# Optimization experiments

Measured on AMD Instinct MI355X. Metric: run time of the kernel, lower is better.

## Reference

```python
import jax, jax.numpy as jnp
import numpy as np
import math

B, H, W = 32, 512, 512
BS = 8
QUALITY = 50.0  # __scale_quality(75) = 200 - 2*75


def _make_dctmtx(bs=BS):
    m = np.empty((bs, bs), dtype=np.float32)
    for j in range(bs):
        for i in range(bs):
            if i == 0:
                m[i, j] = 1.0 / math.sqrt(bs)
            else:
                m[i, j] = math.sqrt(2.0 / bs) * math.cos(math.pi * (2 * j + 1) * i / (2 * bs))
    return jnp.asarray(m)


def _make_quantize():
    qY = np.array([[16,11,10,16,24,40,51,61],[12,12,14,19,26,58,60,55],
                   [14,13,16,24,40,57,69,56],[14,17,22,29,51,87,80,62],
                   [18,22,37,56,68,109,103,77],[24,35,55,64,81,104,113,92],
                   [49,64,78,87,103,121,120,101],[72,92,95,98,112,100,103,99]], dtype=np.float32) / 255.0
    qC = np.array([[17,18,24,47,99,99,99,99],[18,21,26,66,99,99,99,99],
                   [24,26,56,99,99,99,99,99],[47,66,99,99,99,99,99,99],
                   [99,99,99,99,99,99,99,99],[99,99,99,99,99,99,99,99],
                   [99,99,99,99,99,99,99,99],[99,99,99,99,99,99,99,99]], dtype=np.float32) / 255.0
    return jnp.asarray(np.stack([qY, qC, qC], axis=0))


def setup_inputs() -> dict:
    key = jax.random.key(0)
    x = jax.random.uniform(key, (B, 3, H, W), dtype=jnp.float32)
    return {"input": x, "quantize": _make_quantize(), "dctmtx": _make_dctmtx()}


def reference(input, quantize, dctmtx):
    bs = BS
    b, c, h, w = input.shape
    dt = input.dtype
    rgb = 255.0 * input
    # rgb -> ycbcr (3x3 color transform, offset cb/cr by 128, clamp)
    xf = jnp.array([[0.299, 0.587, 0.114],
                    [-0.168735892, -0.331264108, 0.5],
                    [0.5, -0.418687589, -0.081312411]], dtype=dt)
    off = jnp.array([0.0, 128.0, 128.0], dtype=dt)[None, :, None, None]
    ycbcr = jnp.clip(jnp.einsum('bchw,kc->bkhw', rgb, xf) + off, 0.0, 255.0)
    # 2x2 chroma subsample: replace Cb/Cr by 2x2 block means (Y untouched)
    yc = ycbcr[:, :1]
    cc = ycbcr[:, 1:].reshape(b, 2, h // 2, 2, w // 2, 2)
    cm = jnp.mean(cc, axis=(3, 5), keepdims=True)
    cc = jnp.broadcast_to(cm, cc.shape).reshape(b, 2, h, w)
    sample = jnp.concatenate([yc, cc], axis=1) - 128.0
    # extract 8x8 blocks -> [b, h/bs, w/bs, 3, bs, bs]
    blocks = sample.reshape(b, 3, h // bs, bs, w // bs, bs).transpose(0, 2, 4, 1, 3, 5)
    # 2D DCT: D @ X @ D^T
    dcts = jnp.einsum('ij,bhwcjk,lk->bhwcil', dctmtx, blocks, dctmtx)
    # quality-scaled quant table (broadcasts [3,8,8] over blocks)
    q = jnp.round(jnp.clip(jnp.round((jnp.round(quantize * 255.0) * QUALITY + 50.0) / 100.0), 1.0, 255.0))
    comp = jnp.round(dcts / q)
    decomp = jnp.round(comp * jax.lax.stop_gradient(q))
    # IDCT: D^T @ X @ D
    idcts = jnp.einsum('ji,bhwcjk,kl->bhwcil', dctmtx, decomp, dctmtx)
    # merge blocks back -> [b,3,h,w]
    ycbcr2 = idcts.transpose(0, 3, 1, 4, 2, 5).reshape(b, 3, h, w) + 128.0
    # ycbcr -> rgb
    xf2 = jnp.array([[1.0, 0.0, 1.402],
                     [1.0, -0.344136286, -0.714136286],
                     [1.0, 1.772, 0.0]], dtype=dt)
    im = ycbcr2 - off
    rgb2 = jnp.clip(jnp.einsum('bchw,kc->bkhw', im, xf2), 0.0, 255.0)
    return jnp.round(rgb2) / 255.0
```

## Files before the change

kernel.cpp:

```cpp
#include <hip/hip_runtime.h>

#define IN_H 512
#define IN_W 512


__global__ __launch_bounds__(256, 2) void jpeg_kernel(
    const float* __restrict__ in, const float* __restrict__ qz,
    const float* __restrict__ dmtx, float* __restrict__ out)
{
    __shared__ __align__(16) unsigned char smem[39168];
    double*  Ys  = (double*) (smem);
    double*  CbS = (double*) (smem + 17408);
    double*  CrS = (double*) (smem + 22016);
    float*   Zt  = (float*)  (smem + 26624);
    double2* qt  = (double2*)(smem + 35328);
    double*  Dd  = (double*) (smem + 38784);
    float*   Dh  = (float*)  (smem + 39040);

    const int t   = threadIdx.x;
    const int blk = blockIdx.x;
    const int b   = blk >> 7;
    const int rr  = blk & 127;
    const int row0 = (rr >> 1) << 3;
    const int col0 = (rr & 1) << 8;
    const int chs = IN_H * IN_W;

    if (t < 192) {
        const int c = t >> 6, i = (t >> 3) & 7, l = t & 7;
        double v  = (double)qz[t];
        double t1 = rint((rint(v * 255.0) * 50.0 + 50.0) / 100.0);
        double q  = fmin(fmax(t1, 1.0), 255.0);
        qt[(c * 8 + l) * 9 + i] = make_double2(1.0 / q, q);
    }
    if (t < 32) {
        float dv = dmtx[(t >> 2) * 8 + (t & 3)];
        Dd[t] = (double)dv;
        Dh[t] = dv;
    }

    const int s  = t >> 6;
    const int c4 = t & 63;
    {
        const int base = ((b * 3) * IN_H + row0 + 2 * s) * IN_W + col0 + 4 * c4;
        float4 ra = *(const float4*)(in + base);
        float4 rb = *(const float4*)(in + base + IN_W);
        float4 ga = *(const float4*)(in + base + chs);
        float4 gb = *(const float4*)(in + base + chs + IN_W);
        float4 ba = *(const float4*)(in + base + 2 * chs);
        float4 bb = *(const float4*)(in + base + 2 * chs + IN_W);

        float rA[2][4] = {{ra.x,ra.y,ra.z,ra.w},{rb.x,rb.y,rb.z,rb.w}};
        float gA[2][4] = {{ga.x,ga.y,ga.z,ga.w},{gb.x,gb.y,gb.z,gb.w}};
        float bA[2][4] = {{ba.x,ba.y,ba.z,ba.w},{bb.x,bb.y,bb.z,bb.w}};

        double yv[2][4], cbv[2][4], crv[2][4];
        #pragma unroll
        for (int p = 0; p < 2; ++p) {
            #pragma unroll
            for (int k = 0; k < 4; ++k) {
                double R = 255.0 * (double)rA[p][k];
                double G = 255.0 * (double)gA[p][k];
                double B = 255.0 * (double)bA[p][k];
                double y  =  0.299*R + 0.587*G + 0.114*B;
                double cb = -0.168735892*R - 0.331264108*G + 0.5*B + 128.0;
                double cr =  0.5*R - 0.418687589*G - 0.081312411*B + 128.0;
                yv[p][k]  = fmin(fmax(y , 0.0), 255.0) - 128.0;
                cbv[p][k] = fmin(fmax(cb, 0.0), 255.0);
                crv[p][k] = fmin(fmax(cr, 0.0), 255.0);
            }
        }
        const int tile = c4 >> 1, half = c4 & 1;
        #pragma unroll
        for (int p = 0; p < 2; ++p) {
            double* yp = &Ys[tile * 68 + (2*s + p) * 8 + 4 * half];
            *(double2*)(yp)     = make_double2(yv[p][0], yv[p][1]);
            *(double2*)(yp + 2) = make_double2(yv[p][2], yv[p][3]);
        }
        double m0 = (cbv[0][0]+cbv[0][1]+cbv[1][0]+cbv[1][1])*0.25 - 128.0;
        double m1 = (cbv[0][2]+cbv[0][3]+cbv[1][2]+cbv[1][3])*0.25 - 128.0;
        *(double2*)&CbS[tile * 18 + s * 4 + 2 * half] = make_double2(m0, m1);
        double n0 = (crv[0][0]+crv[0][1]+crv[1][0]+crv[1][1])*0.25 - 128.0;
        double n1 = (crv[0][2]+crv[0][3]+crv[1][2]+crv[1][3])*0.25 - 128.0;
        *(double2*)&CrS[tile * 18 + s * 4 + 2 * half] = make_double2(n0, n1);
    }
    __syncthreads();

    const int q8 = t >> 3;
    const int l  = t & 7;
    double dl0, dl1, dl2, dl3;
    {
        double2 dA = *(const double2*)&Dd[l * 4];
        double2 dB = *(const double2*)&Dd[l * 4 + 2];
        dl0 = dA.x; dl1 = dA.y; dl2 = dB.x; dl3 = dB.y;
    }
    const double sgn  = (l & 1) ? -1.0 : 1.0;
    const double dl01 = dl0 + dl1, dl23 = dl2 + dl3;
    float dcol[8];
    {
        const int   lc = (l < 4) ? l : 7 - l;
        #pragma unroll
        for (int k = 0; k < 8; ++k) {
            float dv = Dh[k * 4 + lc];
            dcol[k] = ((k & 1) && (l >= 4)) ? -dv : dv;
        }
    }

    float acc[3][8];

    #pragma unroll
    for (int c = 0; c < 3; ++c) {
        double e2[4], o2[4];
        if (c == 0) {
            const double* base = &Ys[q8 * 68];
            #pragma unroll
            for (int m = 0; m < 4; ++m) {
                double tp[2];
                #pragma unroll
                for (int h = 0; h < 2; ++h) {
                    const double* p = base + (h ? (7 - m) : m) * 8;
                    double2 a0 = *(const double2*)(p);
                    double2 a1 = *(const double2*)(p + 2);
                    double2 a2 = *(const double2*)(p + 4);
                    double2 a3 = *(const double2*)(p + 6);
                    double v0 = fma(sgn, a3.y, a0.x);
                    double v1 = fma(sgn, a3.x, a0.y);
                    double v2 = fma(sgn, a2.y, a1.x);
                    double v3 = fma(sgn, a2.x, a1.y);
                    tp[h] = dl0*v0 + dl1*v1 + dl2*v2 + dl3*v3;
                }
                e2[m] = tp[0] + tp[1];
                o2[m] = tp[0] - tp[1];
            }
        } else {
            const double* base = ((c == 1) ? CbS : CrS) + q8 * 18;
            double u[4];
            #pragma unroll
            for (int j2 = 0; j2 < 4; ++j2) {
                double2 a0 = *(const double2*)(base + j2 * 4);
                double2 a1 = *(const double2*)(base + j2 * 4 + 2);
                u[j2] = dl01 * fma(sgn, a1.y, a0.x) + dl23 * fma(sgn, a1.x, a0.y);
            }
            e2[0] = e2[1] = u[0] + u[3];  o2[0] = o2[1] = u[0] - u[3];
            e2[2] = e2[3] = u[1] + u[2];  o2[2] = o2[3] = u[1] - u[2];
        }

        const double2* dd2  = (const double2*)Dd;
        const double2* qrow = &qt[(c * 8 + l) * 9];
        float* zp = &Zt[q8 * 68 + l * 8];
        #pragma unroll
        for (int hh = 0; hh < 2; ++hh) {
            float zo[4];
            #pragma unroll
            for (int ii = 0; ii < 4; ++ii) {
                const int i = hh * 4 + ii;
                double2 dA = dd2[i * 2], dB = dd2[i * 2 + 1];
                double a64 = (i & 1)
                    ? dA.x*o2[0] + dA.y*o2[1] + dB.x*o2[2] + dB.y*o2[3]
                    : dA.x*e2[0] + dA.y*e2[1] + dB.x*e2[2] + dB.y*e2[3];
                double2 qe = qrow[i];
                zo[ii] = (float)(rint(a64 * qe.x) * qe.y);
            }
            *(float4*)(zp + 4 * hh) = make_float4(zo[0], zo[1], zo[2], zo[3]);
        }
        __syncthreads();

        float w[8] = {0,0,0,0,0,0,0,0};
        const float* zb = &Zt[q8 * 68];
        #pragma unroll
        for (int k = 0; k < 8; ++k) {
            float4 z0 = *(const float4*)(zb + k * 8);
            float4 z1 = *(const float4*)(zb + k * 8 + 4);
            float dk = dcol[k];
            w[0] += z0.x*dk; w[1] += z0.y*dk; w[2] += z0.z*dk; w[3] += z0.w*dk;
            w[4] += z1.x*dk; w[5] += z1.y*dk; w[6] += z1.z*dk; w[7] += z1.w*dk;
        }
        const float4* dh4 = (const float4*)Dh;
        float se[4] = {0,0,0,0}, so[4] = {0,0,0,0};
        #pragma unroll
        for (int j = 0; j < 8; j += 2) {
            float4 de = dh4[j], dq = dh4[j + 1];
            se[0] += de.x*w[j];   se[1] += de.y*w[j];   se[2] += de.z*w[j];   se[3] += de.w*w[j];
            so[0] += dq.x*w[j+1]; so[1] += dq.y*w[j+1]; so[2] += dq.z*w[j+1]; so[3] += dq.w*w[j+1];
        }
        #pragma unroll
        for (int i2 = 0; i2 < 4; ++i2) {
            acc[c][i2]     = se[i2] + so[i2];
            acc[c][7 - i2] = se[i2] - so[i2];
        }
        if (c < 2) __syncthreads();
    }

    #pragma unroll
    for (int i = 0; i < 8; ++i) {
        float im0 = acc[0][i] + 128.0f;
        float im1 = acc[1][i];
        float im2 = acc[2][i];
        float R  = fminf(fmaxf(im0 + 1.402f*im2, 0.0f), 255.0f);
        float G  = fminf(fmaxf(im0 - 0.344136286f*im1 - 0.714136286f*im2, 0.0f), 255.0f);
        float Bv = fminf(fmaxf(im0 + 1.772f*im1, 0.0f), 255.0f);
        const int base = ((b * 3) * IN_H + row0 + i) * IN_W + col0 + t;
        out[base]           = rintf(R)  * (1.0f/255.0f);
        out[base + chs]     = rintf(G)  * (1.0f/255.0f);
        out[base + 2*chs]   = rintf(Bv) * (1.0f/255.0f);
    }
}

extern "C" void kernel_launch(void* const* d_in, const int* in_sizes, int n_in,
                              void* d_out, int out_size, void* d_ws, size_t ws_size,
                              hipStream_t stream) {
    (void)in_sizes; (void)n_in; (void)out_size; (void)d_ws; (void)ws_size;
    const float* in  = (const float*)d_in[0];
    const float* qz  = (const float*)d_in[1];
    const float* dm  = (const float*)d_in[2];
    float* out = (float*)d_out;
    dim3 grid(4096), blk(256);
    hipLaunchKernelGGL(jpeg_kernel, grid, blk, 0, stream, in, qz, dm, out);
}
```

Baseline: 187.2 us.

## Keep IDCT per 8x8 tile within one wave and vectorize output stores

```diff
diff --git a/kernel.cpp b/kernel.cpp
--- a/kernel.cpp
+++ b/kernel.cpp
@@ -12,7 +12,7 @@
     double*  Ys  = (double*) (smem);
     double*  CbS = (double*) (smem + 17408);
     double*  CrS = (double*) (smem + 22016);
-    float*   Zt  = (float*)  (smem + 26624);
+    float*   Vt  = (float*)  (smem + 26624);
     double2* qt  = (double2*)(smem + 35328);
     double*  Dd  = (double*) (smem + 38784);
     float*   Dh  = (float*)  (smem + 39040);
@@ -95,17 +95,12 @@
     }
     const double sgn  = (l & 1) ? -1.0 : 1.0;
     const double dl01 = dl0 + dl1, dl23 = dl2 + dl3;
-    float dcol[8];
-    {
-        const int   lc = (l < 4) ? l : 7 - l;
-        #pragma unroll
-        for (int k = 0; k < 8; ++k) {
-            float dv = Dh[k * 4 + lc];
-            dcol[k] = ((k & 1) && (l >= 4)) ? -dv : dv;
-        }
-    }
+    const float4* dh4p = (const float4*)Dh;
+    float4 d0 = dh4p[0], d1 = dh4p[1], d2 = dh4p[2], d3 = dh4p[3];
+    float4 d4 = dh4p[4], d5 = dh4p[5], d6 = dh4p[6], d7 = dh4p[7];
 
     float acc[3][8];
+    float* vtw = &Vt[q8 * 68];
 
     #pragma unroll
     for (int c = 0; c < 3; ++c) {
@@ -133,75 +128,98 @@
             }
         } else {
             const double* base = ((c == 1) ? CbS : CrS) + q8 * 18;
-            double u[4];
+            double u4[4];
             #pragma unroll
             for (int j2 = 0; j2 < 4; ++j2) {
                 double2 a0 = *(const double2*)(base + j2 * 4);
                 double2 a1 = *(const double2*)(base + j2 * 4 + 2);
-                u[j2] = dl01 * fma(sgn, a1.y, a0.x) + dl23 * fma(sgn, a1.x, a0.y);
-            }
-            e2[0] = e2[1] = u[0] + u[3];  o2[0] = o2[1] = u[0] - u[3];
-            e2[2] = e2[3] = u[1] + u[2];  o2[2] = o2[3] = u[1] - u[2];
-        }
-
-        const double2* dd2  = (const double2*)Dd;
-        const double2* qrow = &qt[(c * 8 + l) * 9];
-        float* zp = &Zt[q8 * 68 + l * 8];
-        #pragma unroll
-        for (int hh = 0; hh < 2; ++hh) {
-            float zo[4];
-            #pragma unroll
-            for (int ii = 0; ii < 4; ++ii) {
-                const int i = hh * 4 + ii;
+                u4[j2] = dl01 * fma(sgn, a1.y, a0.x) + dl23 * fma(sgn, a1.x, a0.y);
+            }
+            e2[0] = e2[1] = u4[0] + u4[3];  o2[0] = o2[1] = u4[0] - u4[3];
+            e2[2] = e2[3] = u4[1] + u4[2];  o2[2] = o2[3] = u4[1] - u4[2];
+        }
+
+        float zo[8];
+        {
+            const double2* dd2  = (const double2*)Dd;
+            const double2* qrow = &qt[(c * 8 + l) * 9];
+            #pragma unroll
+            for (int i = 0; i < 8; ++i) {
                 double2 dA = dd2[i * 2], dB = dd2[i * 2 + 1];
                 double a64 = (i & 1)
                     ? dA.x*o2[0] + dA.y*o2[1] + dB.x*o2[2] + dB.y*o2[3]
                     : dA.x*e2[0] + dA.y*e2[1] + dB.x*e2[2] + dB.y*e2[3];
                 double2 qe = qrow[i];
-                zo[ii] = (float)(rint(a64 * qe.x) * qe.y);
-            }
-            *(float4*)(zp + 4 * hh) = make_float4(zo[0], zo[1], zo[2], zo[3]);
-        }
-        __syncthreads();
-
-        float w[8] = {0,0,0,0,0,0,0,0};
-        const float* zb = &Zt[q8 * 68];
-        #pragma unroll
-        for (int k = 0; k < 8; ++k) {
-            float4 z0 = *(const float4*)(zb + k * 8);
-            float4 z1 = *(const float4*)(zb + k * 8 + 4);
-            float dk = dcol[k];
-            w[0] += z0.x*dk; w[1] += z0.y*dk; w[2] += z0.z*dk; w[3] += z0.w*dk;
-            w[4] += z1.x*dk; w[5] += z1.y*dk; w[6] += z1.z*dk; w[7] += z1.w*dk;
-        }
-        const float4* dh4 = (const float4*)Dh;
-        float se[4] = {0,0,0,0}, so[4] = {0,0,0,0};
-        #pragma unroll
-        for (int j = 0; j < 8; j += 2) {
-            float4 de = dh4[j], dq = dh4[j + 1];
-            se[0] += de.x*w[j];   se[1] += de.y*w[j];   se[2] += de.z*w[j];   se[3] += de.w*w[j];
-            so[0] += dq.x*w[j+1]; so[1] += dq.y*w[j+1]; so[2] += dq.z*w[j+1]; so[3] += dq.w*w[j+1];
-        }
-        #pragma unroll
-        for (int i2 = 0; i2 < 4; ++i2) {
-            acc[c][i2]     = se[i2] + so[i2];
-            acc[c][7 - i2] = se[i2] - so[i2];
-        }
-        if (c < 2) __syncthreads();
-    }
-
-    #pragma unroll
-    for (int i = 0; i < 8; ++i) {
-        float im0 = acc[0][i] + 128.0f;
-        float im1 = acc[1][i];
-        float im2 = acc[2][i];
-        float R  = fminf(fmaxf(im0 + 1.402f*im2, 0.0f), 255.0f);
-        float G  = fminf(fmaxf(im0 - 0.344136286f*im1 - 0.714136286f*im2, 0.0f), 255.0f);
-        float Bv = fminf(fmaxf(im0 + 1.772f*im1, 0.0f), 255.0f);
-        const int base = ((b * 3) * IN_H + row0 + i) * IN_W + col0 + t;
-        out[base]           = rintf(R)  * (1.0f/255.0f);
-        out[base + chs]     = rintf(G)  * (1.0f/255.0f);
-        out[base + 2*chs]   = rintf(Bv) * (1.0f/255.0f);
+                zo[i] = (float)(rint(a64 * qe.x) * qe.y);
+            }
+        }
+
+        float u[8];
+        {
+            float se0 = zo[0]*d0.x + zo[2]*d2.x + zo[4]*d4.x + zo[6]*d6.x;
+            float se1 = zo[0]*d0.y + zo[2]*d2.y + zo[4]*d4.y + zo[6]*d6.y;
+            float se2 = zo[0]*d0.z + zo[2]*d2.z + zo[4]*d4.z + zo[6]*d6.z;
+            float se3 = zo[0]*d0.w + zo[2]*d2.w + zo[4]*d4.w + zo[6]*d6.w;
+            float so0 = zo[1]*d1.x + zo[3]*d3.x + zo[5]*d5.x + zo[7]*d7.x;
+            float so1 = zo[1]*d1.y + zo[3]*d3.y + zo[5]*d5.y + zo[7]*d7.y;
+            float so2 = zo[1]*d1.z + zo[3]*d3.z + zo[5]*d5.z + zo[7]*d7.z;
+            float so3 = zo[1]*d1.w + zo[3]*d3.w + zo[5]*d5.w + zo[7]*d7.w;
+            u[0]=se0+so0; u[7]=se0-so0;
+            u[1]=se1+so1; u[6]=se1-so1;
+            u[2]=se2+so2; u[5]=se2-so2;
+            u[3]=se3+so3; u[4]=se3-so3;
+        }
+
+        #pragma unroll
+        for (int x = 0; x < 8; ++x) vtw[x * 8 + l] = u[x];
+        __builtin_amdgcn_wave_barrier();
+        float w2[8];
+        {
+            const float* vr = vtw + l * 8;
+            float4 wa = *(const float4*)(vr);
+            float4 wb = *(const float4*)(vr + 4);
+            w2[0]=wa.x; w2[1]=wa.y; w2[2]=wa.z; w2[3]=wa.w;
+            w2[4]=wb.x; w2[5]=wb.y; w2[6]=wb.z; w2[7]=wb.w;
+        }
+        __builtin_amdgcn_wave_barrier();
+
+        {
+            float re0 = w2[0]*d0.x + w2[2]*d2.x + w2[4]*d4.x + w2[6]*d6.x;
+            float re1 = w2[0]*d0.y + w2[2]*d2.y + w2[4]*d4.y + w2[6]*d6.y;
+            float re2 = w2[0]*d0.z + w2[2]*d2.z + w2[4]*d4.z + w2[6]*d6.z;
+            float re3 = w2[0]*d0.w + w2[2]*d2.w + w2[4]*d4.w + w2[6]*d6.w;
+            float ro0 = w2[1]*d1.x + w2[3]*d3.x + w2[5]*d5.x + w2[7]*d7.x;
+            float ro1 = w2[1]*d1.y + w2[3]*d3.y + w2[5]*d5.y + w2[7]*d7.y;
+            float ro2 = w2[1]*d1.z + w2[3]*d3.z + w2[5]*d5.z + w2[7]*d7.z;
+            float ro3 = w2[1]*d1.w + w2[3]*d3.w + w2[5]*d5.w + w2[7]*d7.w;
+            acc[c][0]=re0+ro0; acc[c][7]=re0-ro0;
+            acc[c][1]=re1+ro1; acc[c][6]=re1-ro1;
+            acc[c][2]=re2+ro2; acc[c][5]=re2-ro2;
+            acc[c][3]=re3+ro3; acc[c][4]=re3-ro3;
+        }
+    }
+
+    {
+        const int obase = ((b * 3) * IN_H + row0 + l) * IN_W + col0 + q8 * 8;
+        float R4[8], G4[8], B4[8];
+        #pragma unroll
+        for (int y = 0; y < 8; ++y) {
+            float im0 = acc[0][y] + 128.0f;
+            float im1 = acc[1][y];
+            float im2 = acc[2][y];
+            float R  = fminf(fmaxf(im0 + 1.402f*im2, 0.0f), 255.0f);
+            float G  = fminf(fmaxf(im0 - 0.344136286f*im1 - 0.714136286f*im2, 0.0f), 255.0f);
+            float Bv = fminf(fmaxf(im0 + 1.772f*im1, 0.0f), 255.0f);
+            R4[y] = rintf(R)  * (1.0f/255.0f);
+            G4[y] = rintf(G)  * (1.0f/255.0f);
+            B4[y] = rintf(Bv) * (1.0f/255.0f);
+        }
+        *(float4*)(out + obase)               = make_float4(R4[0],R4[1],R4[2],R4[3]);
+        *(float4*)(out + obase + 4)           = make_float4(R4[4],R4[5],R4[6],R4[7]);
+        *(float4*)(out + obase + chs)         = make_float4(G4[0],G4[1],G4[2],G4[3]);
+        *(float4*)(out + obase + chs + 4)     = make_float4(G4[4],G4[5],G4[6],G4[7]);
+        *(float4*)(out + obase + 2*chs)       = make_float4(B4[0],B4[1],B4[2],B4[3]);
+        *(float4*)(out + obase + 2*chs + 4)   = make_float4(B4[4],B4[5],B4[6],B4[7]);
     }
 }
 
```

Measured after the change: 185.1 us. About the same (-1.2%).
